# Performance work log

Measured on AMD Instinct MI355X. Metric: run time of the kernel, lower is better.

## Reference

```python
import jax, jax.numpy as jnp
import numpy as np

N = 50000      # nodes
E = 500000     # edges
F_IN = 128     # num_features
H = 128        # hidden_dim
G = 256        # graphs in batch


def setup_inputs() -> dict:
    key = jax.random.key(0)
    ks = jax.random.split(key, 12)
    x = jax.random.normal(ks[0], (N, F_IN), jnp.float32)
    edge_index = jax.random.randint(ks[1], (2, E), 0, N, dtype=jnp.int32)
    edge_attr = jax.random.uniform(ks[2], (E,), jnp.float32)  # positive edge weights
    batch = jnp.sort(jax.random.randint(ks[3], (N,), 0, G, dtype=jnp.int32))
    s_in = 1.0 / np.sqrt(F_IN)
    s_h = 1.0 / np.sqrt(H)
    return {
        "x": x,
        "edge_index": edge_index,
        "edge_attr": edge_attr,
        "batch": batch,
        "W1": jax.random.normal(ks[4], (H, F_IN), jnp.float32) * s_in,
        "b1": jnp.zeros((H,), jnp.float32),
        "W2": jax.random.normal(ks[5], (H, H), jnp.float32) * s_h,
        "b2": jnp.zeros((H,), jnp.float32),
        "fW1": jax.random.normal(ks[6], (H, H), jnp.float32) * s_h,
        "fb1": jnp.zeros((H,), jnp.float32),
        "fW2": jax.random.normal(ks[7], (1, H), jnp.float32) * s_h,
        "fb2": jnp.zeros((1,), jnp.float32),
    }


def gcn_conv(x, src, dst, ew, W, b, n):
    """PyG GCNConv: linear transform, add self-loops (weight 1),
    symmetric deg^-1/2 normalization with edge weights, scatter-add, bias."""
    h = x @ W.T                                   # [n, H]
    loop = jnp.arange(n, dtype=src.dtype)
    s = jnp.concatenate([src, loop])
    d = jnp.concatenate([dst, loop])
    w = jnp.concatenate([ew, jnp.ones((n,), x.dtype)])
    deg = jax.ops.segment_sum(w, d, num_segments=n)  # weighted in-degree incl. self-loop
    dinv = jnp.where(deg > 0, jax.lax.rsqrt(deg), 0.0)
    norm = dinv[s] * w * dinv[d]                  # [E+n]
    msg = h[s] * norm[:, None]                    # gather + scale: [E+n, H]
    out = jax.ops.segment_sum(msg, d, num_segments=n)  # scatter-add
    return out + b


def reference(x, edge_index, edge_attr, batch, W1, b1, W2, b2, fW1, fb1, fW2, fb2):
    src, dst = edge_index[0], edge_index[1]
    h = jax.nn.relu(gcn_conv(x, src, dst, edge_attr, W1, b1, N))
    h = jax.nn.relu(gcn_conv(h, src, dst, edge_attr, W2, b2, N))
    # global_mean_pool over graph ids
    sums = jax.ops.segment_sum(h, batch, num_segments=G)            # [G, H]
    counts = jax.ops.segment_sum(jnp.ones((N,), h.dtype), batch, num_segments=G)
    pooled = sums / jnp.maximum(counts, 1.0)[:, None]
    o = jax.nn.relu(pooled @ fW1.T + fb1)
    return o @ fW2.T + fb2                                          # [G, 1]
```

## Files before the change

kernel.cpp:

```cpp
#include <hip/hip_runtime.h>
#include <hip/hip_bf16.h>


#define CAP 64
#define CDS 8

typedef __attribute__((ext_vector_type(8))) short short8;
typedef __attribute__((ext_vector_type(4))) float floatx4;

__device__ inline unsigned short f2bf(float f) {
    unsigned int u = __float_as_uint(f);
    u += 0x7FFF + ((u >> 16) & 1);
    return (unsigned short)(u >> 16);
}
__device__ inline float bf2f(unsigned short h) {
    return __uint_as_float(((unsigned int)h) << 16);
}

#define PW 136
__global__ __launch_bounds__(256) void gemm1_build(const float* __restrict__ X,
        const float* __restrict__ W, unsigned short* __restrict__ C, int M,
        const int* __restrict__ src, const int* __restrict__ dst,
        const float* __restrict__ ew, unsigned long long* __restrict__ cd,
        unsigned int* __restrict__ csr, int E, int gemmB) {
    if ((int)blockIdx.x >= gemmB) {
        int i = ((int)blockIdx.x - gemmB) * 256 + (int)threadIdx.x;
        if (i < E) {
            int d = dst[i];
            float w = ew[i];
            unsigned long long pk = (1ULL << 32) |
                                    (unsigned long long)__float2uint_rn(w * 16777216.0f);
            unsigned long long old = atomicAdd(&cd[(size_t)d * CDS], pk);
            int pos = (int)(old >> 32);
            if (pos < CAP)
                csr[((size_t)d << 6) + pos] =
                    ((unsigned int)src[i] << 16) | __float2uint_rn(w * 65535.0f);
        }
        return;
    }

    __shared__ unsigned short whi[128 * PW];
    __shared__ unsigned short wlo[128 * PW];
    const int t = threadIdx.x;

    {
        int j = t >> 1;
        int c0 = (t & 1) * 64;
        const floatx4* wr = (const floatx4*)(W + (size_t)j * 128 + c0);
        unsigned short* dh = &whi[j * PW + c0];
        unsigned short* dl = &wlo[j * PW + c0];
#pragma unroll
        for (int i = 0; i < 16; ++i) {
            floatx4 v = wr[i];
            ushort4 hv, lv;
            hv.x = f2bf(v.x); lv.x = f2bf(v.x - bf2f(hv.x));
            hv.y = f2bf(v.y); lv.y = f2bf(v.y - bf2f(hv.y));
            hv.z = f2bf(v.z); lv.z = f2bf(v.z - bf2f(hv.z));
            hv.w = f2bf(v.w); lv.w = f2bf(v.w - bf2f(hv.w));
            *(ushort4*)(dh + i * 4) = hv;
            *(ushort4*)(dl + i * 4) = lv;
        }
    }
    __syncthreads();

    const int wave = t >> 6;
    const int lane = t & 63;
    const int q = lane >> 4;
    const int ln = lane & 15;
    const int rowbase = blockIdx.x * 128 + wave * 32;

    floatx4 acc[2][8];
#pragma unroll
    for (int s = 0; s < 2; ++s)
#pragma unroll
        for (int ct = 0; ct < 8; ++ct) acc[s][ct] = (floatx4){0.f, 0.f, 0.f, 0.f};

#pragma unroll
    for (int ks = 0; ks < 4; ++ks) {
        short8 ahi[2], alo[2];
#pragma unroll
        for (int s = 0; s < 2; ++s) {
            int row = rowbase + s * 16 + ln;
            int rowc = (row < M) ? row : (M - 1);
            const floatx4* xr = (const floatx4*)(X + (size_t)rowc * 128 + ks * 32 + q * 8);
            floatx4 x0 = xr[0];
            floatx4 x1 = xr[1];
            unsigned short h, l;
            h = f2bf(x0.x); l = f2bf(x0.x - bf2f(h)); ahi[s][0] = (short)h; alo[s][0] = (short)l;
            h = f2bf(x0.y); l = f2bf(x0.y - bf2f(h)); ahi[s][1] = (short)h; alo[s][1] = (short)l;
            h = f2bf(x0.z); l = f2bf(x0.z - bf2f(h)); ahi[s][2] = (short)h; alo[s][2] = (short)l;
            h = f2bf(x0.w); l = f2bf(x0.w - bf2f(h)); ahi[s][3] = (short)h; alo[s][3] = (short)l;
            h = f2bf(x1.x); l = f2bf(x1.x - bf2f(h)); ahi[s][4] = (short)h; alo[s][4] = (short)l;
            h = f2bf(x1.y); l = f2bf(x1.y - bf2f(h)); ahi[s][5] = (short)h; alo[s][5] = (short)l;
            h = f2bf(x1.z); l = f2bf(x1.z - bf2f(h)); ahi[s][6] = (short)h; alo[s][6] = (short)l;
            h = f2bf(x1.w); l = f2bf(x1.w - bf2f(h)); ahi[s][7] = (short)h; alo[s][7] = (short)l;
        }
#pragma unroll
        for (int ct = 0; ct < 8; ++ct) {
            int lidx = (ct * 16 + ln) * PW + ks * 32 + q * 8;
            short8 bhi = *(const short8*)&whi[lidx];
            short8 blo = *(const short8*)&wlo[lidx];
#pragma unroll
            for (int s = 0; s < 2; ++s) {
                acc[s][ct] = __builtin_amdgcn_mfma_f32_16x16x32_bf16(ahi[s], bhi, acc[s][ct], 0, 0, 0);
                acc[s][ct] = __builtin_amdgcn_mfma_f32_16x16x32_bf16(ahi[s], blo, acc[s][ct], 0, 0, 0);
                acc[s][ct] = __builtin_amdgcn_mfma_f32_16x16x32_bf16(alo[s], bhi, acc[s][ct], 0, 0, 0);
            }
        }
    }

#pragma unroll
    for (int s = 0; s < 2; ++s) {
#pragma unroll
        for (int r = 0; r < 4; ++r) {
            int row = rowbase + s * 16 + q * 4 + r;
            if (row < M) {
                unsigned short* cr = C + (size_t)row * 128 + ln;
#pragma unroll
                for (int ct = 0; ct < 8; ++ct) cr[ct * 16] = f2bf(acc[s][ct][r]);
            }
        }
    }
}

__global__ __launch_bounds__(256) void compute_dinv(const unsigned long long* __restrict__ cd,
        float* __restrict__ dinv, int n) {
    int i = blockIdx.x * 256 + threadIdx.x;
    if (i < n) {
        unsigned int lo = (unsigned int)cd[(size_t)i * CDS];
        dinv[i] = rsqrtf((float)lo * 5.9604644775e-8f + 1.0f);
    }
}

__global__ __launch_bounds__(256) void gemm_bf16_nt(const unsigned short* __restrict__ X,
        const float* __restrict__ W, unsigned short* __restrict__ C, int M) {
    __shared__ unsigned short whi[128 * PW];
    __shared__ unsigned short wlo[128 * PW];
    const int t = threadIdx.x;

    {
        int j = t >> 1;
        int c0 = (t & 1) * 64;
        const floatx4* wr = (const floatx4*)(W + (size_t)j * 128 + c0);
        unsigned short* dh = &whi[j * PW + c0];
        unsigned short* dl = &wlo[j * PW + c0];
#pragma unroll
        for (int i = 0; i < 16; ++i) {
            floatx4 v = wr[i];
            ushort4 hv, lv;
            hv.x = f2bf(v.x); lv.x = f2bf(v.x - bf2f(hv.x));
            hv.y = f2bf(v.y); lv.y = f2bf(v.y - bf2f(hv.y));
            hv.z = f2bf(v.z); lv.z = f2bf(v.z - bf2f(hv.z));
            hv.w = f2bf(v.w); lv.w = f2bf(v.w - bf2f(hv.w));
            *(ushort4*)(dh + i * 4) = hv;
            *(ushort4*)(dl + i * 4) = lv;
        }
    }
    __syncthreads();

    const int wave = t >> 6;
    const int lane = t & 63;
    const int q = lane >> 4;
    const int ln = lane & 15;
    const int rowbase = blockIdx.x * 128 + wave * 32;

    floatx4 acc[2][8];
#pragma unroll
    for (int s = 0; s < 2; ++s)
#pragma unroll
        for (int ct = 0; ct < 8; ++ct) acc[s][ct] = (floatx4){0.f, 0.f, 0.f, 0.f};

#pragma unroll
    for (int ks = 0; ks < 4; ++ks) {
        short8 a[2];
#pragma unroll
        for (int s = 0; s < 2; ++s) {
            int row = rowbase + s * 16 + ln;
            int rowc = (row < M) ? row : (M - 1);
            a[s] = *(const short8*)(X + (size_t)rowc * 128 + ks * 32 + q * 8);
        }
#pragma unroll
        for (int ct = 0; ct < 8; ++ct) {
            int lidx = (ct * 16 + ln) * PW + ks * 32 + q * 8;
            short8 bhi = *(const short8*)&whi[lidx];
            short8 blo = *(const short8*)&wlo[lidx];
#pragma unroll
            for (int s = 0; s < 2; ++s) {
                acc[s][ct] = __builtin_amdgcn_mfma_f32_16x16x32_bf16(a[s], bhi, acc[s][ct], 0, 0, 0);
                acc[s][ct] = __builtin_amdgcn_mfma_f32_16x16x32_bf16(a[s], blo, acc[s][ct], 0, 0, 0);
            }
        }
    }

#pragma unroll
    for (int s = 0; s < 2; ++s) {
#pragma unroll
        for (int r = 0; r < 4; ++r) {
            int row = rowbase + s * 16 + q * 4 + r;
            if (row < M) {
                unsigned short* cr = C + (size_t)row * 128 + ln;
#pragma unroll
                for (int ct = 0; ct < 8; ++ct) cr[ct * 16] = f2bf(acc[s][ct][r]);
            }
        }
    }
}

#define UNPACK_W(e) ((float)((e) & 0xFFFFu) * (1.0f / 65535.0f))

__global__ __launch_bounds__(256) void aggregate_finalize(
        const unsigned short* __restrict__ h, const unsigned short* __restrict__ hlin,
        const unsigned long long* __restrict__ cd, const unsigned int* __restrict__ csr,
        const float* __restrict__ dinv, const float* __restrict__ bias,
        unsigned short* __restrict__ outb, int n) {
    int node = blockIdx.x * 8 + (threadIdx.x >> 5);
    if (node >= n) return;
    int lane = threadIdx.x & 31;
    float di = dinv[node];
    float sl = di * di;
    float4 b4 = ((const float4*)bias)[lane];
    ushort4 bse = ((const ushort4*)(hlin + (size_t)node * 128))[lane];
    float4 acc = make_float4(0.f, 0.f, 0.f, 0.f);

    const unsigned int* b = csr + ((size_t)node << 6);
    const uint4* bv = (const uint4*)b;
    int c = (int)(cd[(size_t)node * CDS] >> 32);
    if (c > CAP) c = CAP;
    int k = 0;
    for (; k + 4 <= c; k += 4) {
        uint4 ev = bv[k >> 2];
        int s0 = ev.x >> 16, s1 = ev.y >> 16, s2 = ev.z >> 16, s3 = ev.w >> 16;
        float w0 = UNPACK_W(ev.x) * dinv[s0];
        float w1 = UNPACK_W(ev.y) * dinv[s1];
        float w2 = UNPACK_W(ev.z) * dinv[s2];
        float w3 = UNPACK_W(ev.w) * dinv[s3];
        ushort4 h0 = ((const ushort4*)(h + (size_t)s0 * 128))[lane];
        ushort4 h1 = ((const ushort4*)(h + (size_t)s1 * 128))[lane];
        ushort4 h2 = ((const ushort4*)(h + (size_t)s2 * 128))[lane];
        ushort4 h3 = ((const ushort4*)(h + (size_t)s3 * 128))[lane];
        acc.x += bf2f(h0.x) * w0 + bf2f(h1.x) * w1 + bf2f(h2.x) * w2 + bf2f(h3.x) * w3;
        acc.y += bf2f(h0.y) * w0 + bf2f(h1.y) * w1 + bf2f(h2.y) * w2 + bf2f(h3.y) * w3;
        acc.z += bf2f(h0.z) * w0 + bf2f(h1.z) * w1 + bf2f(h2.z) * w2 + bf2f(h3.z) * w3;
        acc.w += bf2f(h0.w) * w0 + bf2f(h1.w) * w1 + bf2f(h2.w) * w2 + bf2f(h3.w) * w3;
    }
    for (; k < c; ++k) {
        unsigned int e0 = b[k];
        int s0 = e0 >> 16;
        float w = UNPACK_W(e0) * dinv[s0];
        ushort4 hv = ((const ushort4*)(h + (size_t)s0 * 128))[lane];
        acc.x += bf2f(hv.x) * w;
        acc.y += bf2f(hv.y) * w;
        acc.z += bf2f(hv.z) * w;
        acc.w += bf2f(hv.w) * w;
    }
    ushort4 o;
    o.x = f2bf(fmaxf(acc.x * di + bf2f(bse.x) * sl + b4.x, 0.0f));
    o.y = f2bf(fmaxf(acc.y * di + bf2f(bse.y) * sl + b4.y, 0.0f));
    o.z = f2bf(fmaxf(acc.z * di + bf2f(bse.z) * sl + b4.z, 0.0f));
    o.w = f2bf(fmaxf(acc.w * di + bf2f(bse.w) * sl + b4.w, 0.0f));
    ((ushort4*)(outb + (size_t)node * 128))[lane] = o;
}

__global__ __launch_bounds__(256) void aggregate_pool(
        const unsigned short* __restrict__ h,
        const unsigned long long* __restrict__ cd, const unsigned int* __restrict__ csr,
        const float* __restrict__ dinv, const float* __restrict__ bias,
        const int* __restrict__ batch, float* __restrict__ pooled, int n) {
    int slot = threadIdx.x >> 5;
    int node = blockIdx.x * 8 + slot;
    int lane = threadIdx.x & 31;
    __shared__ float red[8][128];
    __shared__ int grp[8];

    float4 o = make_float4(0.f, 0.f, 0.f, 0.f);
    int g = -1;
    if (node < n) {
        g = batch[node];
        float di = dinv[node];
        float sl = di * di;
        float4 b4 = ((const float4*)bias)[lane];
        ushort4 bse = ((const ushort4*)(h + (size_t)node * 128))[lane];
        float4 acc = make_float4(0.f, 0.f, 0.f, 0.f);

        const unsigned int* b = csr + ((size_t)node << 6);
        const uint4* bv = (const uint4*)b;
        int c = (int)(cd[(size_t)node * CDS] >> 32);
        if (c > CAP) c = CAP;
        int k = 0;
        for (; k + 4 <= c; k += 4) {
            uint4 ev = bv[k >> 2];
            int s0 = ev.x >> 16, s1 = ev.y >> 16, s2 = ev.z >> 16, s3 = ev.w >> 16;
            float w0 = UNPACK_W(ev.x) * dinv[s0];
            float w1 = UNPACK_W(ev.y) * dinv[s1];
            float w2 = UNPACK_W(ev.z) * dinv[s2];
            float w3 = UNPACK_W(ev.w) * dinv[s3];
            ushort4 h0 = ((const ushort4*)(h + (size_t)s0 * 128))[lane];
            ushort4 h1 = ((const ushort4*)(h + (size_t)s1 * 128))[lane];
            ushort4 h2 = ((const ushort4*)(h + (size_t)s2 * 128))[lane];
            ushort4 h3 = ((const ushort4*)(h + (size_t)s3 * 128))[lane];
            acc.x += bf2f(h0.x) * w0 + bf2f(h1.x) * w1 + bf2f(h2.x) * w2 + bf2f(h3.x) * w3;
            acc.y += bf2f(h0.y) * w0 + bf2f(h1.y) * w1 + bf2f(h2.y) * w2 + bf2f(h3.y) * w3;
            acc.z += bf2f(h0.z) * w0 + bf2f(h1.z) * w1 + bf2f(h2.z) * w2 + bf2f(h3.z) * w3;
            acc.w += bf2f(h0.w) * w0 + bf2f(h1.w) * w1 + bf2f(h2.w) * w2 + bf2f(h3.w) * w3;
        }
        for (; k < c; ++k) {
            unsigned int e0 = b[k];
            int s0 = e0 >> 16;
            float w = UNPACK_W(e0) * dinv[s0];
            ushort4 hv = ((const ushort4*)(h + (size_t)s0 * 128))[lane];
            acc.x += bf2f(hv.x) * w;
            acc.y += bf2f(hv.y) * w;
            acc.z += bf2f(hv.z) * w;
            acc.w += bf2f(hv.w) * w;
        }
        o.x = fmaxf(acc.x * di + bf2f(bse.x) * sl + b4.x, 0.0f);
        o.y = fmaxf(acc.y * di + bf2f(bse.y) * sl + b4.y, 0.0f);
        o.z = fmaxf(acc.z * di + bf2f(bse.z) * sl + b4.z, 0.0f);
        o.w = fmaxf(acc.w * di + bf2f(bse.w) * sl + b4.w, 0.0f);
    }
    if (lane == 0) grp[slot] = g;
    *(float4*)&red[slot][lane * 4] = o;
    __syncthreads();

    if (threadIdx.x < 128) {
        int j = threadIdx.x;
        float s = 0.f;
        int cg = -1;
#pragma unroll
        for (int r = 0; r < 8; ++r) {
            int gr = grp[r];
            if (gr != cg) {
                if (cg >= 0) atomicAdd(&pooled[(size_t)cg * 128 + j], s);
                s = 0.f;
                cg = gr;
            }
            if (gr >= 0) s += red[r][j];
        }
        if (cg >= 0) atomicAdd(&pooled[(size_t)cg * 128 + j], s);
    }
}

__global__ __launch_bounds__(128) void head_mlp(const float* __restrict__ pooled,
        const int* __restrict__ batch, int n,
        const float* __restrict__ fW1, const float* __restrict__ fb1,
        const float* __restrict__ fW2, const float* __restrict__ fb2,
        float* __restrict__ out) {
    int g = blockIdx.x;
    int j = threadIdx.x;
    int lo = 0, hi = n;
    while (lo < hi) { int mid = (lo + hi) >> 1; if (batch[mid] < g) lo = mid + 1; else hi = mid; }
    int s = lo;
    hi = n;
    while (lo < hi) { int mid = (lo + hi) >> 1; if (batch[mid] < g + 1) lo = mid + 1; else hi = mid; }
    int cnt = lo - s;
    float scale = 1.0f / fmaxf((float)cnt, 1.0f);

    __shared__ float row[128];
    __shared__ float part[2];
    row[j] = pooled[(size_t)g * 128 + j] * scale;
    __syncthreads();
    float acc = fb1[j];
    const float* wr = fW1 + (size_t)j * 128;
#pragma unroll 8
    for (int k = 0; k < 128; ++k) acc += row[k] * wr[k];
    float v = fmaxf(acc, 0.0f) * fW2[j];
#pragma unroll
    for (int off = 32; off > 0; off >>= 1) v += __shfl_down(v, off);
    if ((j & 63) == 0) part[j >> 6] = v;
    __syncthreads();
    if (j == 0) out[g] = part[0] + part[1] + fb2[0];
}

extern "C" void kernel_launch(void* const* d_in, const int* in_sizes, int n_in,
                              void* d_out, int out_size, void* d_ws, size_t ws_size,
                              hipStream_t stream) {
    const float* x   = (const float*)d_in[0];
    const int*   ei  = (const int*)d_in[1];
    const float* ew  = (const float*)d_in[2];
    const int* batch = (const int*)d_in[3];
    const float* W1  = (const float*)d_in[4];
    const float* b1  = (const float*)d_in[5];
    const float* W2  = (const float*)d_in[6];
    const float* b2  = (const float*)d_in[7];
    const float* fW1 = (const float*)d_in[8];
    const float* fb1 = (const float*)d_in[9];
    const float* fW2 = (const float*)d_in[10];
    const float* fb2 = (const float*)d_in[11];
    float* out = (float*)d_out;

    const int N = in_sizes[0] / 128;
    const int E = in_sizes[2];
    const int G = out_size;
    const int* src = ei;
    const int* dst = ei + E;

    unsigned short* A = (unsigned short*)d_ws;
    unsigned short* B = A + (size_t)N * 128;
    unsigned int* csr = (unsigned int*)(B + (size_t)N * 128);
    unsigned long long* cd = (unsigned long long*)(csr + (size_t)N * CAP);
    float* pooled = (float*)(cd + (size_t)N * CDS);
    float* dinv = pooled + (size_t)G * 128;

    const int gemmB = (N + 127) / 128;
    const int buildB = (E + 255) / 256;

    hipMemsetAsync(cd, 0, (size_t)N * CDS * 8 + (size_t)G * 128 * 4, stream);

    gemm1_build<<<gemmB + buildB, 256, 0, stream>>>(x, W1, A, N, src, dst, ew,
                                                    cd, csr, E, gemmB);
    compute_dinv<<<(N + 255) / 256, 256, 0, stream>>>(cd, dinv, N);
    aggregate_finalize<<<(N + 7) / 8, 256, 0, stream>>>(A, A, cd, csr, dinv, b1, B, N);

    gemm_bf16_nt<<<(N + 127) / 128, 256, 0, stream>>>(B, W2, A, N);
    aggregate_pool<<<(N + 7) / 8, 256, 0, stream>>>(A, cd, csr, dinv, b2, batch, pooled, N);

    head_mlp<<<G, 128, 0, stream>>>(pooled, batch, N, fW1, fb1, fW2, fb2, out);
}
```

Baseline: 201.8 us.

## Stripe per-node edge counters four ways and fuse dinv into first GEMM

Edge insertion now spreads each destination's atomics over four counter slots, picked by edge index, and writes into an interleaved four-column CSR bucket with 16 entries per slot. This is meant to cut atomic contention and serialization on hot nodes. The aggregation kernels read the four slot counts and walk the buckets row by row, masking invalid lanes. Masked lanes still issue loads of row 0, so there can be extra wasted gathers when slot counts are uneven. The CSR build is split out of the fused GEMM launch, and the dinv computation is folded into the first GEMM kernel, dropping one launch but giving up the overlap of build and GEMM in one grid.

```diff
diff --git a/kernel.cpp b/kernel.cpp
--- a/kernel.cpp
+++ b/kernel.cpp
@@ -2,7 +2,7 @@
 #include <hip/hip_bf16.h>
 
 
-#define CAP 64
+#define CAP 16
 #define CDS 8
 
 typedef __attribute__((ext_vector_type(8))) short short8;
@@ -17,26 +17,37 @@
     return __uint_as_float(((unsigned int)h) << 16);
 }
 
+__global__ __launch_bounds__(256) void build_csr(const int* __restrict__ src,
+        const int* __restrict__ dst, const float* __restrict__ ew,
+        unsigned long long* __restrict__ cd, unsigned int* __restrict__ csr, int e) {
+    int i = blockIdx.x * blockDim.x + threadIdx.x;
+    if (i < e) {
+        int d = dst[i];
+        float w = ew[i];
+        int r = i & 3;
+        unsigned long long pk = (1ULL << 32) |
+                                (unsigned long long)__float2uint_rn(w * 16777216.0f);
+        unsigned long long old = atomicAdd(&cd[(size_t)d * CDS + r], pk);
+        int pos = (int)(old >> 32);
+        if (pos < CAP)
+            csr[((size_t)d << 6) + pos * 4 + r] =
+                ((unsigned int)src[i] << 16) | __float2uint_rn(w * 65535.0f);
+    }
+}
+
 #define PW 136
-__global__ __launch_bounds__(256) void gemm1_build(const float* __restrict__ X,
-        const float* __restrict__ W, unsigned short* __restrict__ C, int M,
-        const int* __restrict__ src, const int* __restrict__ dst,
-        const float* __restrict__ ew, unsigned long long* __restrict__ cd,
-        unsigned int* __restrict__ csr, int E, int gemmB) {
-    if ((int)blockIdx.x >= gemmB) {
-        int i = ((int)blockIdx.x - gemmB) * 256 + (int)threadIdx.x;
-        if (i < E) {
-            int d = dst[i];
-            float w = ew[i];
-            unsigned long long pk = (1ULL << 32) |
-                                    (unsigned long long)__float2uint_rn(w * 16777216.0f);
-            unsigned long long old = atomicAdd(&cd[(size_t)d * CDS], pk);
-            int pos = (int)(old >> 32);
-            if (pos < CAP)
-                csr[((size_t)d << 6) + pos] =
-                    ((unsigned int)src[i] << 16) | __float2uint_rn(w * 65535.0f);
-        }
-        return;
+__global__ __launch_bounds__(256) void gemm_f32_nt(const float* __restrict__ X,
+        const float* __restrict__ W, unsigned short* __restrict__ C,
+        const unsigned long long* __restrict__ cd, float* __restrict__ dinv, int M) {
+    {
+        int gid = blockIdx.x * 256 + threadIdx.x;
+        if (gid < M) {
+            const uint4* cp = (const uint4*)(cd + (size_t)gid * CDS);
+            uint4 a = cp[0];
+            uint4 b = cp[1];
+            unsigned int s = a.x + a.z + b.x + b.z;
+            dinv[gid] = rsqrtf((float)s * 5.9604644775e-8f + 1.0f);
+        }
     }
 
     __shared__ unsigned short whi[128 * PW];
@@ -123,15 +134,6 @@
     }
 }
 
-__global__ __launch_bounds__(256) void compute_dinv(const unsigned long long* __restrict__ cd,
-        float* __restrict__ dinv, int n) {
-    int i = blockIdx.x * 256 + threadIdx.x;
-    if (i < n) {
-        unsigned int lo = (unsigned int)cd[(size_t)i * CDS];
-        dinv[i] = rsqrtf((float)lo * 5.9604644775e-8f + 1.0f);
-    }
-}
-
 __global__ __launch_bounds__(256) void gemm_bf16_nt(const unsigned short* __restrict__ X,
         const float* __restrict__ W, unsigned short* __restrict__ C, int M) {
     __shared__ unsigned short whi[128 * PW];
@@ -207,6 +209,13 @@
 }
 
 #define UNPACK_W(e) ((float)((e) & 0xFFFFu) * (1.0f / 65535.0f))
+
+#define PROC_ELEM(eraw, valid, hv_, wv_)                                   \
+    {                                                                      \
+        int sx = (valid) ? (int)((eraw) >> 16) : 0;                        \
+        wv_ = (valid) ? UNPACK_W(eraw) * dinv[sx] : 0.0f;                  \
+        hv_ = ((const ushort4*)(h + (size_t)sx * 128))[lane];              \
+    }
 
 __global__ __launch_bounds__(256) void aggregate_finalize(
         const unsigned short* __restrict__ h, const unsigned short* __restrict__ hlin,
@@ -222,36 +231,26 @@
     ushort4 bse = ((const ushort4*)(hlin + (size_t)node * 128))[lane];
     float4 acc = make_float4(0.f, 0.f, 0.f, 0.f);
 
-    const unsigned int* b = csr + ((size_t)node << 6);
-    const uint4* bv = (const uint4*)b;
-    int c = (int)(cd[(size_t)node * CDS] >> 32);
-    if (c > CAP) c = CAP;
-    int k = 0;
-    for (; k + 4 <= c; k += 4) {
-        uint4 ev = bv[k >> 2];
-        int s0 = ev.x >> 16, s1 = ev.y >> 16, s2 = ev.z >> 16, s3 = ev.w >> 16;
-        float w0 = UNPACK_W(ev.x) * dinv[s0];
-        float w1 = UNPACK_W(ev.y) * dinv[s1];
-        float w2 = UNPACK_W(ev.z) * dinv[s2];
-        float w3 = UNPACK_W(ev.w) * dinv[s3];
-        ushort4 h0 = ((const ushort4*)(h + (size_t)s0 * 128))[lane];
-        ushort4 h1 = ((const ushort4*)(h + (size_t)s1 * 128))[lane];
-        ushort4 h2 = ((const ushort4*)(h + (size_t)s2 * 128))[lane];
-        ushort4 h3 = ((const ushort4*)(h + (size_t)s3 * 128))[lane];
+    const uint4* cp = (const uint4*)(cd + (size_t)node * CDS);
+    uint4 ca = cp[0];
+    uint4 cb = cp[1];
+    int c0 = min((int)ca.y, CAP), c1 = min((int)ca.w, CAP);
+    int c2 = min((int)cb.y, CAP), c3 = min((int)cb.w, CAP);
+    int mx = max(max(c0, c1), max(c2, c3));
+
+    const uint4* bv = (const uint4*)(csr + ((size_t)node << 6));
+    for (int p = 0; p < mx; ++p) {
+        uint4 ev = bv[p];
+        ushort4 h0, h1, h2, h3;
+        float w0, w1, w2, w3;
+        PROC_ELEM(ev.x, p < c0, h0, w0);
+        PROC_ELEM(ev.y, p < c1, h1, w1);
+        PROC_ELEM(ev.z, p < c2, h2, w2);
+        PROC_ELEM(ev.w, p < c3, h3, w3);
         acc.x += bf2f(h0.x) * w0 + bf2f(h1.x) * w1 + bf2f(h2.x) * w2 + bf2f(h3.x) * w3;
         acc.y += bf2f(h0.y) * w0 + bf2f(h1.y) * w1 + bf2f(h2.y) * w2 + bf2f(h3.y) * w3;
         acc.z += bf2f(h0.z) * w0 + bf2f(h1.z) * w1 + bf2f(h2.z) * w2 + bf2f(h3.z) * w3;
         acc.w += bf2f(h0.w) * w0 + bf2f(h1.w) * w1 + bf2f(h2.w) * w2 + bf2f(h3.w) * w3;
-    }
-    for (; k < c; ++k) {
-        unsigned int e0 = b[k];
-        int s0 = e0 >> 16;
-        float w = UNPACK_W(e0) * dinv[s0];
-        ushort4 hv = ((const ushort4*)(h + (size_t)s0 * 128))[lane];
-        acc.x += bf2f(hv.x) * w;
-        acc.y += bf2f(hv.y) * w;
-        acc.z += bf2f(hv.z) * w;
-        acc.w += bf2f(hv.w) * w;
     }
     ushort4 o;
     o.x = f2bf(fmaxf(acc.x * di + bf2f(bse.x) * sl + b4.x, 0.0f));
@@ -282,36 +281,26 @@
         ushort4 bse = ((const ushort4*)(h + (size_t)node * 128))[lane];
         float4 acc = make_float4(0.f, 0.f, 0.f, 0.f);
 
-        const unsigned int* b = csr + ((size_t)node << 6);
-        const uint4* bv = (const uint4*)b;
-        int c = (int)(cd[(size_t)node * CDS] >> 32);
-        if (c > CAP) c = CAP;
-        int k = 0;
-        for (; k + 4 <= c; k += 4) {
-            uint4 ev = bv[k >> 2];
-            int s0 = ev.x >> 16, s1 = ev.y >> 16, s2 = ev.z >> 16, s3 = ev.w >> 16;
-            float w0 = UNPACK_W(ev.x) * dinv[s0];
-            float w1 = UNPACK_W(ev.y) * dinv[s1];
-            float w2 = UNPACK_W(ev.z) * dinv[s2];
-            float w3 = UNPACK_W(ev.w) * dinv[s3];
-            ushort4 h0 = ((const ushort4*)(h + (size_t)s0 * 128))[lane];
-            ushort4 h1 = ((const ushort4*)(h + (size_t)s1 * 128))[lane];
-            ushort4 h2 = ((const ushort4*)(h + (size_t)s2 * 128))[lane];
-            ushort4 h3 = ((const ushort4*)(h + (size_t)s3 * 128))[lane];
+        const uint4* cp = (const uint4*)(cd + (size_t)node * CDS);
+        uint4 ca = cp[0];
+        uint4 cb = cp[1];
+        int c0 = min((int)ca.y, CAP), c1 = min((int)ca.w, CAP);
+        int c2 = min((int)cb.y, CAP), c3 = min((int)cb.w, CAP);
+        int mx = max(max(c0, c1), max(c2, c3));
+
+        const uint4* bv = (const uint4*)(csr + ((size_t)node << 6));
+        for (int p = 0; p < mx; ++p) {
+            uint4 ev = bv[p];
+            ushort4 h0, h1, h2, h3;
+            float w0, w1, w2, w3;
+            PROC_ELEM(ev.x, p < c0, h0, w0);
+            PROC_ELEM(ev.y, p < c1, h1, w1);
+            PROC_ELEM(ev.z, p < c2, h2, w2);
+            PROC_ELEM(ev.w, p < c3, h3, w3);
             acc.x += bf2f(h0.x) * w0 + bf2f(h1.x) * w1 + bf2f(h2.x) * w2 + bf2f(h3.x) * w3;
             acc.y += bf2f(h0.y) * w0 + bf2f(h1.y) * w1 + bf2f(h2.y) * w2 + bf2f(h3.y) * w3;
             acc.z += bf2f(h0.z) * w0 + bf2f(h1.z) * w1 + bf2f(h2.z) * w2 + bf2f(h3.z) * w3;
             acc.w += bf2f(h0.w) * w0 + bf2f(h1.w) * w1 + bf2f(h2.w) * w2 + bf2f(h3.w) * w3;
-        }
-        for (; k < c; ++k) {
-            unsigned int e0 = b[k];
-            int s0 = e0 >> 16;
-            float w = UNPACK_W(e0) * dinv[s0];
-            ushort4 hv = ((const ushort4*)(h + (size_t)s0 * 128))[lane];
-            acc.x += bf2f(hv.x) * w;
-            acc.y += bf2f(hv.y) * w;
-            acc.z += bf2f(hv.z) * w;
-            acc.w += bf2f(hv.w) * w;
         }
         o.x = fmaxf(acc.x * di + bf2f(bse.x) * sl + b4.x, 0.0f);
         o.y = fmaxf(acc.y * di + bf2f(bse.y) * sl + b4.y, 0.0f);
@@ -397,18 +386,15 @@
     unsigned short* A = (unsigned short*)d_ws;
     unsigned short* B = A + (size_t)N * 128;
     unsigned int* csr = (unsigned int*)(B + (size_t)N * 128);
-    unsigned long long* cd = (unsigned long long*)(csr + (size_t)N * CAP);
+    unsigned long long* cd = (unsigned long long*)(csr + (size_t)N * 64);
     float* pooled = (float*)(cd + (size_t)N * CDS);
     float* dinv = pooled + (size_t)G * 128;
 
-    const int gemmB = (N + 127) / 128;
-    const int buildB = (E + 255) / 256;
-
     hipMemsetAsync(cd, 0, (size_t)N * CDS * 8 + (size_t)G * 128 * 4, stream);
 
-    gemm1_build<<<gemmB + buildB, 256, 0, stream>>>(x, W1, A, N, src, dst, ew,
-                                                    cd, csr, E, gemmB);
-    compute_dinv<<<(N + 255) / 256, 256, 0, stream>>>(cd, dinv, N);
+    build_csr<<<(E + 255) / 256, 256, 0, stream>>>(src, dst, ew, cd, csr, E);
+
+    gemm_f32_nt<<<(N + 127) / 128, 256, 0, stream>>>(x, W1, A, cd, dinv, N);
     aggregate_finalize<<<(N + 7) / 8, 256, 0, stream>>>(A, A, cd, csr, dinv, b1, B, N);
 
     gemm_bf16_nt<<<(N + 127) / 128, 256, 0, stream>>>(B, W2, A, N);
```

Result: slower. 235.5 us (+16.7%).
